# Optimization experiments

Measured on AMD Instinct MI355X. Metric: run time of the kernel, lower is better.

The kernel has to match this reference:

```python
import jax, jax.numpy as jnp
import numpy as np

P = 3            # spline degree per axis (cubic)
NC = 64          # control points per axis
DOUT = 3         # output dimension of control points
NQ = 1_000_000   # number of query points


def open_uniform_knots(n, p):
    interior = np.linspace(0.0, 1.0, n - p + 1)
    return np.concatenate([np.zeros(p), interior, np.ones(p)]).astype(np.float32)  # len n+p+1


def bspline_basis(t, p, x):
    """Cox-de Boor basis. t:[n+p+1], x:[N] -> (i:[N,p+1] int, b:[N,p+1] float)."""
    n_basis = t.shape[0] - p - 1
    t_clamped = jnp.clip(x, t[p], t[-p - 1])
    k = jnp.searchsorted(t, t_clamped, side='right') - 1
    k = jnp.clip(k, p, n_basis - 1)                       # [N]
    i = k[:, None] + jnp.arange(-p, 1)                    # [N, p+1] global basis idx
    d = jnp.broadcast_to(jnp.eye(p + 1, dtype=x.dtype), (x.shape[0], p + 1, p + 1))
    for r in range(1, p + 1):
        j = jnp.arange(p, r - 1, -1)                      # [p-r+1]
        jk = j[None, :] + k[:, None]                      # [N, p-r+1]
        left = t[jk - p]
        right = t[jk + 1 - r]
        alpha = ((x[:, None] - left) / (right - left))[..., None]  # [N, p-r+1, 1]
        d = d.at[:, j].set((1.0 - alpha) * d[:, j - 1] + alpha * d[:, j])
    return i, d[:, p]                                     # basis values sum to 1


def setup_inputs() -> dict:
    key = jax.random.key(0)
    kq, kc = jax.random.split(key)
    queries = jax.random.uniform(kq, (NQ, 3), dtype=jnp.float32)
    control_points = jax.random.normal(kc, (NC * NC * NC, DOUT), dtype=jnp.float32)
    t = jnp.asarray(open_uniform_knots(NC, P))
    return {"queries": queries, "control_points": control_points,
            "tx": t, "ty": t, "tz": t}


def reference(queries, control_points, tx, ty, tz):
    px = py = pz = P
    ix, bx = bspline_basis(tx, px, queries[:, 0])   # [N,px+1]
    iy, by = bspline_basis(ty, py, queries[:, 1])
    iz, bz = bspline_basis(tz, pz, queries[:, 2])
    nx = tx.shape[0] - px - 1
    ny = ty.shape[0] - py - 1
    # flat index into [nx*ny*nz] control grid: ix + nx*(iy + ny*iz)
    flat_idx = (ix[:, :, None, None]
                + nx * (iy[:, None, :, None] + ny * iz[:, None, None, :]))  # [N,px+1,py+1,pz+1]
    cp_sel = control_points[flat_idx]                   # [N,px+1,py+1,pz+1,DOUT]
    y = jnp.einsum('na,nb,nc,nabcd->nd', bx, by, bz, cp_sel)
    return y
```

## Files before the change

### kernel.cpp

```cpp
#include <hip/hip_runtime.h>


#define NC 64
#define NSEG 61
#define NCELLS 512
#define WDIM 11
#define CAP 2560
#define CHUNK 512
#define NCHUNK 5
#define CHUNK_S 2048
#define OVF_CAP 4096

typedef float vfloat4 __attribute__((ext_vector_type(4)));

__device__ __forceinline__ float rcpf(float x) {
#if __has_builtin(__builtin_amdgcn_rcpf)
  return __builtin_amdgcn_rcpf(x);
#else
  return 1.0f / x;
#endif
}

__device__ __forceinline__ int span_of(float x) {
  float xc = fminf(fmaxf(x, 0.0f), 1.0f);
  int j = (int)floorf(xc * (float)NSEG);
  return j > NSEG - 1 ? NSEG - 1 : (j < 0 ? 0 : j);
}

__device__ __forceinline__ float knotv(int i) {
  float v = (float)(i - 3) * (1.0f / (float)NSEG);
  return fminf(fmaxf(v, 0.0f), 1.0f);
}

__device__ __forceinline__ void basis4(float x, int j, float N[4]) {
  float xc = fminf(fmaxf(x, 0.0f), 1.0f);
  int k = j + 3;
  float left[4], right[4];
  N[0] = 1.0f;
#pragma unroll
  for (int jj = 1; jj <= 3; ++jj) {
    left[jj] = xc - knotv(k + 1 - jj);
    right[jj] = knotv(k + jj) - xc;
    float saved = 0.0f;
#pragma unroll
    for (int r = 0; r < jj; ++r) {
      float temp = N[r] * rcpf(right[r + 1] + left[jj - r]);
      N[r] = saved + right[r + 1] * temp;
      saved = left[jj - r] * temp;
    }
    N[jj] = saved;
  }
}

__device__ __forceinline__ void eval_point(float x, float y, float z, int jx,
                                           int jy, int jz,
                                           const float* __restrict__ cp,
                                           float o[3]) {
  float Nx[4], Ny[4], Nz[4];
  basis4(x, jx, Nx);
  basis4(y, jy, Ny);
  basis4(z, jz, Nz);
  float ax = 0, ay = 0, az = 0;
#pragma unroll 1
  for (int c = 0; c < 4; ++c) {
#pragma unroll
    for (int b = 0; b < 4; ++b) {
      float w = Ny[b] * Nz[c];
      const float* row = cp + 3 * (size_t)(jx + NC * (jy + b + NC * (jz + c)));
      vfloat4 f0, f1, f2;
      __builtin_memcpy(&f0, row + 0, 16);
      __builtin_memcpy(&f1, row + 4, 16);
      __builtin_memcpy(&f2, row + 8, 16);
      ax += w * (Nx[0] * f0.x + Nx[1] * f0.w + Nx[2] * f1.z + Nx[3] * f2.y);
      ay += w * (Nx[0] * f0.y + Nx[1] * f1.x + Nx[2] * f1.w + Nx[3] * f2.z);
      az += w * (Nx[0] * f0.z + Nx[1] * f1.y + Nx[2] * f2.x + Nx[3] * f2.w);
    }
  }
  o[0] = ax; o[1] = ay; o[2] = az;
}

__device__ __forceinline__ void scan512_excl(int* arr) {
  int tid = threadIdx.x;
  int c0 = arr[tid], c1 = arr[tid + 256];
#pragma unroll
  for (int off = 1; off < 512; off <<= 1) {
    int t0 = (tid >= off) ? arr[tid - off] : 0;
    int t1 = ((tid + 256) >= off) ? arr[tid + 256 - off] : 0;
    __syncthreads();
    arr[tid] += t0;
    arr[tid + 256] += t1;
    __syncthreads();
  }
  arr[tid] -= c0;
  arr[tid + 256] -= c1;
  __syncthreads();
}


__global__ __launch_bounds__(256) void scatter_capped(
    const float* __restrict__ q, int* __restrict__ gcursor,
    int* __restrict__ ovfcnt, float4* __restrict__ ovf,
    float4* __restrict__ sorted, int nq) {
  __shared__ int hist[NCELLS];
  __shared__ int gb[NCELLS];
  __shared__ int lcur[NCELLS];
  __shared__ float4 stage[CHUNK_S];
  __shared__ int addr[CHUNK_S];
  int b = blockIdx.x, tid = threadIdx.x;
  for (int c = tid; c < NCELLS; c += 256) { hist[c] = 0; lcur[c] = 0; }
  __syncthreads();

  int s = b * CHUNK_S, e = min(nq, s + CHUNK_S);
  int nblk = e - s;
  float xs[8], ys[8], zs[8];
  int cells[8];
  unsigned us[8];
#pragma unroll
  for (int it = 0; it < 8; ++it) {
    int i = s + it * 256 + tid;
    cells[it] = -1;
    if (i < e) {
      float xyz[3];
      __builtin_memcpy(xyz, q + 3 * (size_t)i, 12);
      xs[it] = xyz[0]; ys[it] = xyz[1]; zs[it] = xyz[2];
      int jx = span_of(xyz[0]), jy = span_of(xyz[1]), jz = span_of(xyz[2]);
      cells[it] = (jx >> 3) + 8 * (jy >> 3) + 64 * (jz >> 3);
      us[it] = (unsigned)i | ((unsigned)(jx & 7) << 20) |
               ((unsigned)(jy & 7) << 23) | ((unsigned)(jz & 7) << 26);
      atomicAdd(&hist[cells[it]], 1);
    }
  }
  __syncthreads();
  int n0 = hist[tid], n1 = hist[tid + 256];
  gb[tid] = n0 ? atomicAdd(&gcursor[tid], n0) : 0;
  gb[tid + 256] = n1 ? atomicAdd(&gcursor[tid + 256], n1) : 0;
  __syncthreads();
  scan512_excl(hist);
#pragma unroll
  for (int it = 0; it < 8; ++it) {
    int cell = cells[it];
    if (cell < 0) continue;
    int rank = atomicAdd(&lcur[cell], 1);
    int rloc = hist[cell] + rank;
    int rg = gb[cell] + rank;
    if (rg < CAP) {
      stage[rloc] = make_float4(xs[it], ys[it], zs[it],
                                __int_as_float((int)us[it]));
      addr[rloc] = cell * CAP + rg;
    } else {
      addr[rloc] = -1;
      int p = atomicAdd(ovfcnt, 1);
      if (p < OVF_CAP)
        ovf[p] = make_float4(xs[it], ys[it], zs[it],
                             __int_as_float((int)(us[it] & 0xFFFFFu)));
    }
  }
  __syncthreads();
  for (int j = tid; j < nblk; j += 256) {
    int a = addr[j];
    if (a >= 0) sorted[a] = stage[j];
  }
}


__global__ __launch_bounds__(256) void eval_kernel(
    const float4* __restrict__ sorted, const int* __restrict__ cellcnt,
    const float* __restrict__ cp, float* __restrict__ out) {
  int cid = blockIdx.x / NCHUNK;
  int chunkid = blockIdx.x % NCHUNK;
  int cnt = min(cellcnt[cid], CAP);
  int q0 = chunkid * CHUNK;
  if (q0 >= cnt) return;
  int n = min(cnt - q0, CHUNK);
  size_t base = (size_t)cid * CAP + q0;
  int ox = (cid & 7) * 8, oy = ((cid >> 3) & 7) * 8, oz = (cid >> 6) * 8;
  int tid = threadIdx.x;

  __shared__ float4 lds[WDIM * WDIM * WDIM];
  __shared__ int bins[CHUNK];
  __shared__ unsigned short order[CHUNK];
  for (int e2 = tid; e2 < WDIM * WDIM * WDIM; e2 += 256) {
    int lx = e2 % WDIM, t = e2 / WDIM;
    int ly = t % WDIM, lz = t / WDIM;
    int gx = min(ox + lx, NC - 1), gy = min(oy + ly, NC - 1),
        gz = min(oz + lz, NC - 1);
    const float* p = cp + 3 * (size_t)(gx + NC * (gy + NC * gz));
    lds[e2] = make_float4(p[0], p[1], p[2], 0.0f);
  }
  bins[tid] = 0;
  bins[tid + 256] = 0;
  int k0 = -1, k1 = -1, r0 = 0, r1 = 0;
  if (tid < n)
    k0 = (int)(((unsigned)__float_as_int(sorted[base + tid].w) >> 20) & 511u);
  if (tid + 256 < n)
    k1 = (int)(((unsigned)__float_as_int(sorted[base + tid + 256].w) >> 20) & 511u);
  __syncthreads();
  if (k0 >= 0) r0 = atomicAdd(&bins[k0], 1);
  if (k1 >= 0) r1 = atomicAdd(&bins[k1], 1);
  __syncthreads();
  scan512_excl(bins);
  if (k0 >= 0) order[bins[k0] + r0] = (unsigned short)tid;
  if (k1 >= 0) order[bins[k1] + r1] = (unsigned short)(tid + 256);
  __syncthreads();

  for (int t2 = tid; t2 < n; t2 += 256) {
    int lidx = order[t2];
    float4 s = sorted[base + lidx];
    unsigned u = (unsigned)__float_as_int(s.w);
    int oi = (int)(u & 0xFFFFFu);
    int lx0 = (int)((u >> 20) & 7), ly0 = (int)((u >> 23) & 7),
        lz0 = (int)((u >> 26) & 7);
    float Nx[4], Ny[4], Nz[4];
    basis4(s.x, ox + lx0, Nx);
    basis4(s.y, oy + ly0, Ny);
    basis4(s.z, oz + lz0, Nz);

    float ax = 0.0f, ay = 0.0f, az = 0.0f;
#pragma unroll
    for (int c = 0; c < 4; ++c) {
#pragma unroll
      for (int b = 0; b < 4; ++b) {
        float w = Ny[b] * Nz[c];
        const float4* row = &lds[((lz0 + c) * WDIM + (ly0 + b)) * WDIM + lx0];
        float4 p0 = row[0], p1 = row[1], p2 = row[2], p3 = row[3];
        ax += w * (Nx[0] * p0.x + Nx[1] * p1.x + Nx[2] * p2.x + Nx[3] * p3.x);
        ay += w * (Nx[0] * p0.y + Nx[1] * p1.y + Nx[2] * p2.y + Nx[3] * p3.y);
        az += w * (Nx[0] * p0.z + Nx[1] * p1.z + Nx[2] * p2.z + Nx[3] * p3.z);
      }
    }
    float o[3] = {ax, ay, az};
    __builtin_memcpy(out + 3 * (size_t)oi, o, 12);
  }
}

__global__ __launch_bounds__(256) void ovf_kernel(const float4* __restrict__ ovf,
                                                  const int* __restrict__ ovfcnt,
                                                  const float* __restrict__ cp,
                                                  float* __restrict__ out) {
  int n = min(*ovfcnt, OVF_CAP);
  for (int i = blockIdx.x * 256 + threadIdx.x; i < n; i += gridDim.x * 256) {
    float4 s = ovf[i];
    int oi = __float_as_int(s.w);
    float o[3];
    eval_point(s.x, s.y, s.z, span_of(s.x), span_of(s.y), span_of(s.z), cp, o);
    __builtin_memcpy(out + 3 * (size_t)oi, o, 12);
  }
}

__global__ __launch_bounds__(256) void spline_direct_kernel(
    const float* __restrict__ q, const float* __restrict__ cp,
    float* __restrict__ out, int nq) {
  int i = blockIdx.x * 256 + threadIdx.x;
  if (i >= nq) return;
  float xyz[3];
  __builtin_memcpy(xyz, q + 3 * (size_t)i, 12);
  float o[3];
  eval_point(xyz[0], xyz[1], xyz[2], span_of(xyz[0]), span_of(xyz[1]),
             span_of(xyz[2]), cp, o);
  __builtin_memcpy(out + 3 * (size_t)i, o, 12);
}

extern "C" void kernel_launch(void* const* d_in, const int* in_sizes, int n_in,
                              void* d_out, int out_size, void* d_ws,
                              size_t ws_size, hipStream_t stream) {
  const float* queries = (const float*)d_in[0];
  const float* control = (const float*)d_in[1];
  float* out = (float*)d_out;
  int nq = in_sizes[0] / 3;

  size_t meta = (NCELLS + 1) * sizeof(int);
  size_t metap = (meta + 15) & ~15ull;
  size_t need = metap + (size_t)OVF_CAP * 16 + (size_t)NCELLS * CAP * 16;

  if (nq <= (1 << 20) && ws_size >= need) {
    int* gcursor = (int*)d_ws;
    int* ovfcnt = gcursor + NCELLS;
    float4* ovf = (float4*)((char*)d_ws + metap);
    float4* sorted = ovf + OVF_CAP;
    hipMemsetAsync(d_ws, 0, meta, stream);
    int nb = (nq + CHUNK_S - 1) / CHUNK_S;
    scatter_capped<<<nb, 256, 0, stream>>>(queries, gcursor, ovfcnt, ovf,
                                           sorted, nq);
    eval_kernel<<<NCELLS * NCHUNK, 256, 0, stream>>>(sorted, gcursor, control,
                                                     out);
    ovf_kernel<<<4, 256, 0, stream>>>(ovf, ovfcnt, control, out);
  } else {
    spline_direct_kernel<<<(nq + 255) / 256, 256, 0, stream>>>(queries, control,
                                                               out, nq);
  }
}
```

Baseline: 135.1 us.

## Replace block-staged scatter with global two-pass counting sort by cell and subkey

```diff
diff --git a/kernel.cpp b/kernel.cpp
--- a/kernel.cpp
+++ b/kernel.cpp
@@ -4,11 +4,11 @@
 #define NC 64
 #define NSEG 61
 #define NCELLS 512
+#define NKEYS 512
 #define WDIM 11
 #define CAP 2560
 #define CHUNK 512
 #define NCHUNK 5
-#define CHUNK_S 2048
 #define OVF_CAP 4096
 
 typedef float vfloat4 __attribute__((ext_vector_type(4)));
@@ -96,72 +96,59 @@
   __syncthreads();
 }
 
-
-__global__ __launch_bounds__(256) void scatter_capped(
-    const float* __restrict__ q, int* __restrict__ gcursor,
+__global__ __launch_bounds__(256) void hist_kernel(const float* __restrict__ q,
+                                                   int* __restrict__ hist,
+                                                   int nq) {
+  int stride = gridDim.x * 256;
+  for (int i = blockIdx.x * 256 + threadIdx.x; i < nq; i += stride) {
+    float xyz[3];
+    __builtin_memcpy(xyz, q + 3 * (size_t)i, 12);
+    int jx = span_of(xyz[0]), jy = span_of(xyz[1]), jz = span_of(xyz[2]);
+    int cell = (jx >> 3) + 8 * (jy >> 3) + 64 * (jz >> 3);
+    int key = (jx & 7) + 8 * (jy & 7) + 64 * (jz & 7);
+    atomicAdd(&hist[cell * NKEYS + key], 1);
+  }
+}
+
+__global__ __launch_bounds__(256) void keyscan_kernel(int* __restrict__ hist,
+                                                      int* __restrict__ cellcnt) {
+  __shared__ int sh[NKEYS];
+  int c = blockIdx.x, tid = threadIdx.x;
+  int base = c * NKEYS;
+  int v1 = hist[base + tid + 256];
+  sh[tid] = hist[base + tid];
+  sh[tid + 256] = v1;
+  __syncthreads();
+  scan512_excl(sh);
+  hist[base + tid] = sh[tid];
+  hist[base + tid + 256] = sh[tid + 256];
+  if (tid == 255) cellcnt[c] = sh[511] + v1;
+}
+
+__global__ __launch_bounds__(256) void scatter_kernel(
+    const float* __restrict__ q, int* __restrict__ off,
     int* __restrict__ ovfcnt, float4* __restrict__ ovf,
     float4* __restrict__ sorted, int nq) {
-  __shared__ int hist[NCELLS];
-  __shared__ int gb[NCELLS];
-  __shared__ int lcur[NCELLS];
-  __shared__ float4 stage[CHUNK_S];
-  __shared__ int addr[CHUNK_S];
-  int b = blockIdx.x, tid = threadIdx.x;
-  for (int c = tid; c < NCELLS; c += 256) { hist[c] = 0; lcur[c] = 0; }
-  __syncthreads();
-
-  int s = b * CHUNK_S, e = min(nq, s + CHUNK_S);
-  int nblk = e - s;
-  float xs[8], ys[8], zs[8];
-  int cells[8];
-  unsigned us[8];
-#pragma unroll
-  for (int it = 0; it < 8; ++it) {
-    int i = s + it * 256 + tid;
-    cells[it] = -1;
-    if (i < e) {
-      float xyz[3];
-      __builtin_memcpy(xyz, q + 3 * (size_t)i, 12);
-      xs[it] = xyz[0]; ys[it] = xyz[1]; zs[it] = xyz[2];
-      int jx = span_of(xyz[0]), jy = span_of(xyz[1]), jz = span_of(xyz[2]);
-      cells[it] = (jx >> 3) + 8 * (jy >> 3) + 64 * (jz >> 3);
-      us[it] = (unsigned)i | ((unsigned)(jx & 7) << 20) |
-               ((unsigned)(jy & 7) << 23) | ((unsigned)(jz & 7) << 26);
-      atomicAdd(&hist[cells[it]], 1);
-    }
-  }
-  __syncthreads();
-  int n0 = hist[tid], n1 = hist[tid + 256];
-  gb[tid] = n0 ? atomicAdd(&gcursor[tid], n0) : 0;
-  gb[tid + 256] = n1 ? atomicAdd(&gcursor[tid + 256], n1) : 0;
-  __syncthreads();
-  scan512_excl(hist);
-#pragma unroll
-  for (int it = 0; it < 8; ++it) {
-    int cell = cells[it];
-    if (cell < 0) continue;
-    int rank = atomicAdd(&lcur[cell], 1);
-    int rloc = hist[cell] + rank;
-    int rg = gb[cell] + rank;
-    if (rg < CAP) {
-      stage[rloc] = make_float4(xs[it], ys[it], zs[it],
-                                __int_as_float((int)us[it]));
-      addr[rloc] = cell * CAP + rg;
+  int stride = gridDim.x * 256;
+  for (int i = blockIdx.x * 256 + threadIdx.x; i < nq; i += stride) {
+    float xyz[3];
+    __builtin_memcpy(xyz, q + 3 * (size_t)i, 12);
+    int jx = span_of(xyz[0]), jy = span_of(xyz[1]), jz = span_of(xyz[2]);
+    int cell = (jx >> 3) + 8 * (jy >> 3) + 64 * (jz >> 3);
+    int key = (jx & 7) + 8 * (jy & 7) + 64 * (jz & 7);
+    int pos = atomicAdd(&off[cell * NKEYS + key], 1);
+    if (pos < CAP) {
+      unsigned u = (unsigned)i | ((unsigned)(jx & 7) << 20) |
+                   ((unsigned)(jy & 7) << 23) | ((unsigned)(jz & 7) << 26);
+      sorted[(size_t)cell * CAP + pos] =
+          make_float4(xyz[0], xyz[1], xyz[2], __int_as_float((int)u));
     } else {
-      addr[rloc] = -1;
       int p = atomicAdd(ovfcnt, 1);
       if (p < OVF_CAP)
-        ovf[p] = make_float4(xs[it], ys[it], zs[it],
-                             __int_as_float((int)(us[it] & 0xFFFFFu)));
-    }
-  }
-  __syncthreads();
-  for (int j = tid; j < nblk; j += 256) {
-    int a = addr[j];
-    if (a >= 0) sorted[a] = stage[j];
-  }
-}
-
+        ovf[p] = make_float4(xyz[0], xyz[1], xyz[2], __int_as_float(i));
+    }
+  }
+}
 
 __global__ __launch_bounds__(256) void eval_kernel(
     const float4* __restrict__ sorted, const int* __restrict__ cellcnt,
@@ -171,14 +158,12 @@
   int cnt = min(cellcnt[cid], CAP);
   int q0 = chunkid * CHUNK;
   if (q0 >= cnt) return;
-  int n = min(cnt - q0, CHUNK);
-  size_t base = (size_t)cid * CAP + q0;
+  int qend = min(cnt, q0 + CHUNK);
+  size_t base = (size_t)cid * CAP;
   int ox = (cid & 7) * 8, oy = ((cid >> 3) & 7) * 8, oz = (cid >> 6) * 8;
   int tid = threadIdx.x;
 
   __shared__ float4 lds[WDIM * WDIM * WDIM];
-  __shared__ int bins[CHUNK];
-  __shared__ unsigned short order[CHUNK];
   for (int e2 = tid; e2 < WDIM * WDIM * WDIM; e2 += 256) {
     int lx = e2 % WDIM, t = e2 / WDIM;
     int ly = t % WDIM, lz = t / WDIM;
@@ -187,25 +172,10 @@
     const float* p = cp + 3 * (size_t)(gx + NC * (gy + NC * gz));
     lds[e2] = make_float4(p[0], p[1], p[2], 0.0f);
   }
-  bins[tid] = 0;
-  bins[tid + 256] = 0;
-  int k0 = -1, k1 = -1, r0 = 0, r1 = 0;
-  if (tid < n)
-    k0 = (int)(((unsigned)__float_as_int(sorted[base + tid].w) >> 20) & 511u);
-  if (tid + 256 < n)
-    k1 = (int)(((unsigned)__float_as_int(sorted[base + tid + 256].w) >> 20) & 511u);
   __syncthreads();
-  if (k0 >= 0) r0 = atomicAdd(&bins[k0], 1);
-  if (k1 >= 0) r1 = atomicAdd(&bins[k1], 1);
-  __syncthreads();
-  scan512_excl(bins);
-  if (k0 >= 0) order[bins[k0] + r0] = (unsigned short)tid;
-  if (k1 >= 0) order[bins[k1] + r1] = (unsigned short)(tid + 256);
-  __syncthreads();
-
-  for (int t2 = tid; t2 < n; t2 += 256) {
-    int lidx = order[t2];
-    float4 s = sorted[base + lidx];
+
+  for (int qi = q0 + tid; qi < qend; qi += 256) {
+    float4 s = sorted[base + qi];
     unsigned u = (unsigned)__float_as_int(s.w);
     int oi = (int)(u & 0xFFFFFu);
     int lx0 = (int)((u >> 20) & 7), ly0 = (int)((u >> 23) & 7),
@@ -268,20 +238,22 @@
   float* out = (float*)d_out;
   int nq = in_sizes[0] / 3;
 
-  size_t meta = (NCELLS + 1) * sizeof(int);
+  size_t meta = ((size_t)NCELLS * NKEYS + 1 + NCELLS) * sizeof(int);
   size_t metap = (meta + 15) & ~15ull;
   size_t need = metap + (size_t)OVF_CAP * 16 + (size_t)NCELLS * CAP * 16;
 
   if (nq <= (1 << 20) && ws_size >= need) {
-    int* gcursor = (int*)d_ws;
-    int* ovfcnt = gcursor + NCELLS;
+    int* hist = (int*)d_ws;
+    int* ovfcnt = hist + (size_t)NCELLS * NKEYS;
+    int* cellcnt = ovfcnt + 1;
     float4* ovf = (float4*)((char*)d_ws + metap);
     float4* sorted = ovf + OVF_CAP;
-    hipMemsetAsync(d_ws, 0, meta, stream);
-    int nb = (nq + CHUNK_S - 1) / CHUNK_S;
-    scatter_capped<<<nb, 256, 0, stream>>>(queries, gcursor, ovfcnt, ovf,
-                                           sorted, nq);
-    eval_kernel<<<NCELLS * NCHUNK, 256, 0, stream>>>(sorted, gcursor, control,
+    hipMemsetAsync(hist, 0, ((size_t)NCELLS * NKEYS + 1) * sizeof(int), stream);
+    hist_kernel<<<1024, 256, 0, stream>>>(queries, hist, nq);
+    keyscan_kernel<<<NCELLS, 256, 0, stream>>>(hist, cellcnt);
+    scatter_kernel<<<1024, 256, 0, stream>>>(queries, hist, ovfcnt, ovf,
+                                             sorted, nq);
+    eval_kernel<<<NCELLS * NCHUNK, 256, 0, stream>>>(sorted, cellcnt, control,
                                                      out);
     ovf_kernel<<<4, 256, 0, stream>>>(ovf, ovfcnt, control, out);
   } else {
```

Measured after the change: 230.0 us. 70.2% more time.

## Evaluate each cell with one 512-thread block and stage sorted points in LDS

Applied to the files above, without the earlier changes.

```diff
diff --git a/kernel.cpp b/kernel.cpp
--- a/kernel.cpp
+++ b/kernel.cpp
@@ -6,8 +6,6 @@
 #define NCELLS 512
 #define WDIM 11
 #define CAP 2560
-#define CHUNK 512
-#define NCHUNK 5
 #define CHUNK_S 2048
 #define OVF_CAP 4096
 
@@ -79,7 +77,7 @@
   o[0] = ax; o[1] = ay; o[2] = az;
 }
 
-__device__ __forceinline__ void scan512_excl(int* arr) {
+__device__ __forceinline__ void scan512_t256(int* arr) {
   int tid = threadIdx.x;
   int c0 = arr[tid], c1 = arr[tid + 256];
 #pragma unroll
@@ -96,6 +94,19 @@
   __syncthreads();
 }
 
+__device__ __forceinline__ void scan512_t512(int* arr) {
+  int tid = threadIdx.x;
+  int c0 = arr[tid];
+#pragma unroll
+  for (int off = 1; off < 512; off <<= 1) {
+    int t0 = (tid >= off) ? arr[tid - off] : 0;
+    __syncthreads();
+    arr[tid] += t0;
+    __syncthreads();
+  }
+  arr[tid] -= c0;
+  __syncthreads();
+}
 
 __global__ __launch_bounds__(256) void scatter_capped(
     const float* __restrict__ q, int* __restrict__ gcursor,
@@ -135,7 +146,7 @@
   gb[tid] = n0 ? atomicAdd(&gcursor[tid], n0) : 0;
   gb[tid + 256] = n1 ? atomicAdd(&gcursor[tid + 256], n1) : 0;
   __syncthreads();
-  scan512_excl(hist);
+  scan512_t256(hist);
 #pragma unroll
   for (int it = 0; it < 8; ++it) {
     int cell = cells[it];
@@ -162,50 +173,53 @@
   }
 }
 
-
-__global__ __launch_bounds__(256) void eval_kernel(
+__global__ __launch_bounds__(512) void eval_kernel(
     const float4* __restrict__ sorted, const int* __restrict__ cellcnt,
     const float* __restrict__ cp, float* __restrict__ out) {
-  int cid = blockIdx.x / NCHUNK;
-  int chunkid = blockIdx.x % NCHUNK;
+  int cid = blockIdx.x;
   int cnt = min(cellcnt[cid], CAP);
-  int q0 = chunkid * CHUNK;
-  if (q0 >= cnt) return;
-  int n = min(cnt - q0, CHUNK);
-  size_t base = (size_t)cid * CAP + q0;
+  if (cnt == 0) return;
+  size_t base = (size_t)cid * CAP;
   int ox = (cid & 7) * 8, oy = ((cid >> 3) & 7) * 8, oz = (cid >> 6) * 8;
   int tid = threadIdx.x;
 
-  __shared__ float4 lds[WDIM * WDIM * WDIM];
-  __shared__ int bins[CHUNK];
-  __shared__ unsigned short order[CHUNK];
-  for (int e2 = tid; e2 < WDIM * WDIM * WDIM; e2 += 256) {
+  __shared__ float4 win[WDIM * WDIM * WDIM];
+  __shared__ float4 stage[CAP];
+  __shared__ int bins[512];
+  for (int e2 = tid; e2 < WDIM * WDIM * WDIM; e2 += 512) {
     int lx = e2 % WDIM, t = e2 / WDIM;
     int ly = t % WDIM, lz = t / WDIM;
     int gx = min(ox + lx, NC - 1), gy = min(oy + ly, NC - 1),
         gz = min(oz + lz, NC - 1);
     const float* p = cp + 3 * (size_t)(gx + NC * (gy + NC * gz));
-    lds[e2] = make_float4(p[0], p[1], p[2], 0.0f);
+    win[e2] = make_float4(p[0], p[1], p[2], 0.0f);
   }
   bins[tid] = 0;
-  bins[tid + 256] = 0;
-  int k0 = -1, k1 = -1, r0 = 0, r1 = 0;
-  if (tid < n)
-    k0 = (int)(((unsigned)__float_as_int(sorted[base + tid].w) >> 20) & 511u);
-  if (tid + 256 < n)
-    k1 = (int)(((unsigned)__float_as_int(sorted[base + tid + 256].w) >> 20) & 511u);
-  __syncthreads();
-  if (k0 >= 0) r0 = atomicAdd(&bins[k0], 1);
-  if (k1 >= 0) r1 = atomicAdd(&bins[k1], 1);
-  __syncthreads();
-  scan512_excl(bins);
-  if (k0 >= 0) order[bins[k0] + r0] = (unsigned short)tid;
-  if (k1 >= 0) order[bins[k1] + r1] = (unsigned short)(tid + 256);
-  __syncthreads();
-
-  for (int t2 = tid; t2 < n; t2 += 256) {
-    int lidx = order[t2];
-    float4 s = sorted[base + lidx];
+
+  float4 pt[5];
+  int key[5], rk[5];
+#pragma unroll
+  for (int it = 0; it < 5; ++it) {
+    int idx = it * 512 + tid;
+    key[it] = -1;
+    if (idx < cnt) {
+      pt[it] = sorted[base + idx];
+      key[it] = (int)((((unsigned)__float_as_int(pt[it].w)) >> 20) & 511u);
+    }
+  }
+  __syncthreads();
+#pragma unroll
+  for (int it = 0; it < 5; ++it)
+    if (key[it] >= 0) rk[it] = atomicAdd(&bins[key[it]], 1);
+  __syncthreads();
+  scan512_t512(bins);
+#pragma unroll
+  for (int it = 0; it < 5; ++it)
+    if (key[it] >= 0) stage[bins[key[it]] + rk[it]] = pt[it];
+  __syncthreads();
+
+  for (int t2 = tid; t2 < cnt; t2 += 512) {
+    float4 s = stage[t2];
     unsigned u = (unsigned)__float_as_int(s.w);
     int oi = (int)(u & 0xFFFFFu);
     int lx0 = (int)((u >> 20) & 7), ly0 = (int)((u >> 23) & 7),
@@ -221,7 +235,7 @@
 #pragma unroll
       for (int b = 0; b < 4; ++b) {
         float w = Ny[b] * Nz[c];
-        const float4* row = &lds[((lz0 + c) * WDIM + (ly0 + b)) * WDIM + lx0];
+        const float4* row = &win[((lz0 + c) * WDIM + (ly0 + b)) * WDIM + lx0];
         float4 p0 = row[0], p1 = row[1], p2 = row[2], p3 = row[3];
         ax += w * (Nx[0] * p0.x + Nx[1] * p1.x + Nx[2] * p2.x + Nx[3] * p3.x);
         ay += w * (Nx[0] * p0.y + Nx[1] * p1.y + Nx[2] * p2.y + Nx[3] * p3.y);
@@ -281,8 +295,7 @@
     int nb = (nq + CHUNK_S - 1) / CHUNK_S;
     scatter_capped<<<nb, 256, 0, stream>>>(queries, gcursor, ovfcnt, ovf,
                                            sorted, nq);
-    eval_kernel<<<NCELLS * NCHUNK, 256, 0, stream>>>(sorted, gcursor, control,
-                                                     out);
+    eval_kernel<<<NCELLS, 512, 0, stream>>>(sorted, gcursor, control, out);
     ovf_kernel<<<4, 256, 0, stream>>>(ovf, ovfcnt, control, out);
   } else {
     spline_direct_kernel<<<(nq + 255) / 256, 256, 0, stream>>>(queries, control,
```

Result: slower. 151.8 us (+12.3%).

## Merge overflow eval into eval kernel, enlarge chunks, coarsen local sort key

Applied to the files above, without the earlier changes.

```diff
diff --git a/kernel.cpp b/kernel.cpp
--- a/kernel.cpp
+++ b/kernel.cpp
@@ -6,8 +6,8 @@
 #define NCELLS 512
 #define WDIM 11
 #define CAP 2560
-#define CHUNK 512
-#define NCHUNK 5
+#define ECHUNK 1024
+#define NCHUNK 3
 #define CHUNK_S 2048
 #define OVF_CAP 4096
 
@@ -79,7 +79,7 @@
   o[0] = ax; o[1] = ay; o[2] = az;
 }
 
-__device__ __forceinline__ void scan512_excl(int* arr) {
+__device__ __forceinline__ void scan512_t256(int* arr) {
   int tid = threadIdx.x;
   int c0 = arr[tid], c1 = arr[tid + 256];
 #pragma unroll
@@ -95,7 +95,6 @@
   arr[tid + 256] -= c1;
   __syncthreads();
 }
-
 
 __global__ __launch_bounds__(256) void scatter_capped(
     const float* __restrict__ q, int* __restrict__ gcursor,
@@ -135,7 +134,7 @@
   gb[tid] = n0 ? atomicAdd(&gcursor[tid], n0) : 0;
   gb[tid + 256] = n1 ? atomicAdd(&gcursor[tid + 256], n1) : 0;
   __syncthreads();
-  scan512_excl(hist);
+  scan512_t256(hist);
 #pragma unroll
   for (int it = 0; it < 8; ++it) {
     int cell = cells[it];
@@ -162,45 +161,71 @@
   }
 }
 
-
 __global__ __launch_bounds__(256) void eval_kernel(
     const float4* __restrict__ sorted, const int* __restrict__ cellcnt,
+    const int* __restrict__ ovfcnt, const float4* __restrict__ ovf,
     const float* __restrict__ cp, float* __restrict__ out) {
+  int tid = threadIdx.x;
+  if (blockIdx.x >= NCELLS * NCHUNK) {
+    int n = min(*ovfcnt, OVF_CAP);
+    for (int i = tid; i < n; i += 256) {
+      float4 s = ovf[i];
+      int oi = __float_as_int(s.w);
+      float o[3];
+      eval_point(s.x, s.y, s.z, span_of(s.x), span_of(s.y), span_of(s.z), cp, o);
+      __builtin_memcpy(out + 3 * (size_t)oi, o, 12);
+    }
+    return;
+  }
   int cid = blockIdx.x / NCHUNK;
   int chunkid = blockIdx.x % NCHUNK;
   int cnt = min(cellcnt[cid], CAP);
-  int q0 = chunkid * CHUNK;
+  int q0 = chunkid * ECHUNK;
   if (q0 >= cnt) return;
-  int n = min(cnt - q0, CHUNK);
+  int n = min(cnt - q0, ECHUNK);
   size_t base = (size_t)cid * CAP + q0;
   int ox = (cid & 7) * 8, oy = ((cid >> 3) & 7) * 8, oz = (cid >> 6) * 8;
-  int tid = threadIdx.x;
-
-  __shared__ float4 lds[WDIM * WDIM * WDIM];
-  __shared__ int bins[CHUNK];
-  __shared__ unsigned short order[CHUNK];
+
+  __shared__ float4 win[WDIM * WDIM * WDIM];
+  __shared__ int bins[64];
+  __shared__ unsigned short order[ECHUNK];
   for (int e2 = tid; e2 < WDIM * WDIM * WDIM; e2 += 256) {
     int lx = e2 % WDIM, t = e2 / WDIM;
     int ly = t % WDIM, lz = t / WDIM;
     int gx = min(ox + lx, NC - 1), gy = min(oy + ly, NC - 1),
         gz = min(oz + lz, NC - 1);
     const float* p = cp + 3 * (size_t)(gx + NC * (gy + NC * gz));
-    lds[e2] = make_float4(p[0], p[1], p[2], 0.0f);
-  }
-  bins[tid] = 0;
-  bins[tid + 256] = 0;
-  int k0 = -1, k1 = -1, r0 = 0, r1 = 0;
-  if (tid < n)
-    k0 = (int)(((unsigned)__float_as_int(sorted[base + tid].w) >> 20) & 511u);
-  if (tid + 256 < n)
-    k1 = (int)(((unsigned)__float_as_int(sorted[base + tid + 256].w) >> 20) & 511u);
-  __syncthreads();
-  if (k0 >= 0) r0 = atomicAdd(&bins[k0], 1);
-  if (k1 >= 0) r1 = atomicAdd(&bins[k1], 1);
-  __syncthreads();
-  scan512_excl(bins);
-  if (k0 >= 0) order[bins[k0] + r0] = (unsigned short)tid;
-  if (k1 >= 0) order[bins[k1] + r1] = (unsigned short)(tid + 256);
+    win[e2] = make_float4(p[0], p[1], p[2], 0.0f);
+  }
+  if (tid < 64) bins[tid] = 0;
+  int key[4], rk[4];
+#pragma unroll
+  for (int it = 0; it < 4; ++it) {
+    int idx = it * 256 + tid;
+    key[it] = -1;
+    if (idx < n)
+      key[it] =
+          (int)(((unsigned)__float_as_int(sorted[base + idx].w) >> 23) & 63u);
+  }
+  __syncthreads();
+#pragma unroll
+  for (int it = 0; it < 4; ++it)
+    if (key[it] >= 0) rk[it] = atomicAdd(&bins[key[it]], 1);
+  __syncthreads();
+  if (tid < 64) {
+    int v = bins[tid], incl = v;
+#pragma unroll
+    for (int off = 1; off < 64; off <<= 1) {
+      int t = __shfl_up(incl, off, 64);
+      if (tid >= off) incl += t;
+    }
+    bins[tid] = incl - v;
+  }
+  __syncthreads();
+#pragma unroll
+  for (int it = 0; it < 4; ++it)
+    if (key[it] >= 0)
+      order[bins[key[it]] + rk[it]] = (unsigned short)(it * 256 + tid);
   __syncthreads();
 
   for (int t2 = tid; t2 < n; t2 += 256) {
@@ -221,7 +246,7 @@
 #pragma unroll
       for (int b = 0; b < 4; ++b) {
         float w = Ny[b] * Nz[c];
-        const float4* row = &lds[((lz0 + c) * WDIM + (ly0 + b)) * WDIM + lx0];
+        const float4* row = &win[((lz0 + c) * WDIM + (ly0 + b)) * WDIM + lx0];
         float4 p0 = row[0], p1 = row[1], p2 = row[2], p3 = row[3];
         ax += w * (Nx[0] * p0.x + Nx[1] * p1.x + Nx[2] * p2.x + Nx[3] * p3.x);
         ay += w * (Nx[0] * p0.y + Nx[1] * p1.y + Nx[2] * p2.y + Nx[3] * p3.y);
@@ -229,20 +254,6 @@
       }
     }
     float o[3] = {ax, ay, az};
-    __builtin_memcpy(out + 3 * (size_t)oi, o, 12);
-  }
-}
-
-__global__ __launch_bounds__(256) void ovf_kernel(const float4* __restrict__ ovf,
-                                                  const int* __restrict__ ovfcnt,
-                                                  const float* __restrict__ cp,
-                                                  float* __restrict__ out) {
-  int n = min(*ovfcnt, OVF_CAP);
-  for (int i = blockIdx.x * 256 + threadIdx.x; i < n; i += gridDim.x * 256) {
-    float4 s = ovf[i];
-    int oi = __float_as_int(s.w);
-    float o[3];
-    eval_point(s.x, s.y, s.z, span_of(s.x), span_of(s.y), span_of(s.z), cp, o);
     __builtin_memcpy(out + 3 * (size_t)oi, o, 12);
   }
 }
@@ -281,9 +292,9 @@
     int nb = (nq + CHUNK_S - 1) / CHUNK_S;
     scatter_capped<<<nb, 256, 0, stream>>>(queries, gcursor, ovfcnt, ovf,
                                            sorted, nq);
-    eval_kernel<<<NCELLS * NCHUNK, 256, 0, stream>>>(sorted, gcursor, control,
-                                                     out);
-    ovf_kernel<<<4, 256, 0, stream>>>(ovf, ovfcnt, control, out);
+    eval_kernel<<<NCELLS * NCHUNK + 1, 256, 0, stream>>>(sorted, gcursor,
+                                                         ovfcnt, ovf, control,
+                                                         out);
   } else {
     spline_direct_kernel<<<(nq + 255) / 256, 256, 0, stream>>>(queries, control,
                                                                out, nq);
```

Result: slower. 138.2 us (+2.3%).
